# Kernel tuning notes

Measured on AMD Instinct MI355X. Metric: run time of the kernel, lower is better.

The kernel has to match this reference:

```python
import jax, jax.numpy as jnp
import numpy as np

B, S, DIM, HID = 2, 256, 128, 128
EPS = 1e-5

def _ln(t, w, b):
    mu = jnp.mean(t, axis=-1, keepdims=True)
    var = jnp.mean(jnp.square(t - mu), axis=-1, keepdims=True)
    return (t - mu) * jax.lax.rsqrt(var + EPS) * w + b

def setup_inputs() -> dict:
    key = jax.random.key(0)
    ks = jax.random.split(key, 8)
    sc = 1.0 / np.sqrt(DIM)
    return {
        "x": jax.random.normal(ks[0], (B, S, S, DIM), dtype=jnp.float32),
        "mask": jax.random.uniform(ks[1], (B, S, S), dtype=jnp.float32),
        "norm_w": jnp.ones((DIM,), jnp.float32),
        "norm_b": jnp.zeros((DIM,), jnp.float32),
        "w_left": jax.random.uniform(ks[2], (HID, DIM), jnp.float32, -sc, sc),
        "w_right": jax.random.uniform(ks[3], (HID, DIM), jnp.float32, -sc, sc),
        "w_lg": jax.random.uniform(ks[4], (HID, DIM), jnp.float32, -sc, sc),
        "w_rg": jax.random.uniform(ks[5], (HID, DIM), jnp.float32, -sc, sc),
        "w_og": jax.random.uniform(ks[6], (HID, DIM), jnp.float32, -sc, sc),
        "out_norm_w": jnp.ones((HID,), jnp.float32),
        "out_norm_b": jnp.zeros((HID,), jnp.float32),
        "w_out": jax.random.uniform(ks[7], (DIM, HID), jnp.float32, -1.0 / np.sqrt(HID), 1.0 / np.sqrt(HID)),
    }

def reference(x, mask, norm_w, norm_b, w_left, w_right, w_lg, w_rg, w_og,
              out_norm_w, out_norm_b, w_out):
    xn = _ln(x, norm_w, norm_b)                      # [B,S,S,D]
    m = mask[..., None]                              # [B,S,S,1]
    left = (xn @ w_left.T) * m * jax.nn.sigmoid(xn @ w_lg.T)    # [B,S,S,H]
    right = (xn @ w_right.T) * m * jax.nn.sigmoid(xn @ w_rg.T)  # [B,S,S,H]
    out_gate = jax.nn.sigmoid(xn @ w_og.T)
    # torch: permute to [B,H,S,S], bf16 bmm, permute back -> out[b,i,j,h] = sum_k L[b,i,k,h]*R[b,j,k,h]
    out = jnp.einsum("bikh,bjkh->bijh",
                     left.astype(jnp.bfloat16), right.astype(jnp.bfloat16),
                     preferred_element_type=jnp.float32)
    out = out.astype(jnp.bfloat16).astype(jnp.float32)
    out = _ln(out, out_norm_w, out_norm_b) * out_gate
    return out @ w_out.T                             # [B,S,S,D]
```

## Files before the change

kernel.cpp:

```cpp
#include <hip/hip_runtime.h>


#define SS 256
#define DD 128
#define HH 128

typedef __attribute__((ext_vector_type(8))) short bf16x8;
typedef __attribute__((ext_vector_type(4))) float f32x4;

__device__ __forceinline__ unsigned short f2b(float f) {
  unsigned u = __builtin_bit_cast(unsigned, f);
  u = (u + 0x7FFFu + ((u >> 16) & 1u)) >> 16;
  return (unsigned short)u;
}
__device__ __forceinline__ float b2f(unsigned short h) {
  return __builtin_bit_cast(float, ((unsigned)h) << 16);
}
__device__ __forceinline__ float sigmoidf_(float x) {
  return 1.0f / (1.0f + expf(-x));
}

__global__ __launch_bounds__(1024) void k_cvt(
    const float* __restrict__ s0, const float* __restrict__ s1,
    const float* __restrict__ s2, const float* __restrict__ s3,
    const float* __restrict__ s4, const float* __restrict__ s5,
    unsigned short* __restrict__ dst)
{
  int m = blockIdx.x >> 4;
  int e = ((blockIdx.x & 15) << 10) | threadIdx.x;
  const float* s = (m == 0) ? s0 : (m == 1) ? s1 : (m == 2) ? s2
                 : (m == 3) ? s3 : (m == 4) ? s4 : s5;
  dst[m * 16384 + e] = f2b(s[e]);
}

__global__ __launch_bounds__(256, 4) void k_stage1(
    const float* __restrict__ x, const float* __restrict__ mask,
    const float* __restrict__ nw, const float* __restrict__ nb,
    const unsigned short* __restrict__ wb,
    unsigned short* __restrict__ Lt, unsigned short* __restrict__ Rt,
    unsigned short* __restrict__ og)
{
  __shared__ unsigned short xnS[64][136];
  __shared__ unsigned short oS[128][72];
  __shared__ float maskS[64];

  const int tid  = threadIdx.x;
  const int wave = tid >> 6, lane = tid & 63;
  const int quad = lane >> 4, l16 = lane & 15;
  const int r0 = blockIdx.x * 64;
  const int bq = r0 >> 16, iq = (r0 >> 8) & 255, j0 = r0 & 255;

  if (tid < 64) maskS[tid] = mask[r0 + tid];

  const float w0 = nw[lane], w1 = nw[lane + 64];
  const float b0 = nb[lane], b1 = nb[lane + 64];
  float v0a[16], v1a[16];
  #pragma unroll
  for (int rr = 0; rr < 16; ++rr) {
    const float* xr = x + (size_t)(r0 + wave * 16 + rr) * DD;
    v0a[rr] = xr[lane];
    v1a[rr] = xr[lane + 64];
  }
  #pragma unroll
  for (int rr = 0; rr < 16; ++rr) {
    int r = wave * 16 + rr;
    float v0 = v0a[rr], v1 = v1a[rr];
    float s = v0 + v1;
    #pragma unroll
    for (int o = 32; o; o >>= 1) s += __shfl_xor(s, o);
    float mu = s * (1.0f / 128.0f);
    float d0 = v0 - mu, d1 = v1 - mu;
    float q = d0 * d0 + d1 * d1;
    #pragma unroll
    for (int o = 32; o; o >>= 1) q += __shfl_xor(q, o);
    float rs = rsqrtf(q * (1.0f / 128.0f) + 1e-5f);
    xnS[r][lane]      = f2b(d0 * rs * w0 + b0);
    xnS[r][lane + 64] = f2b(d1 * rs * w1 + b1);
  }
  __syncthreads();

  const int h0 = wave * 32;
  const int jl = quad * 4;

  auto coopStore = [&](unsigned short* dstBase) {
    int h = tid >> 1, half = tid & 1;
    const bf16x8* s = (const bf16x8*)&oS[h][half * 32];
    bf16x8* d = (bf16x8*)(dstBase +
        ((((size_t)bq * 128 + h) * 256 + iq) * 256 + j0 + half * 32));
    d[0] = s[0]; d[1] = s[1]; d[2] = s[2]; d[3] = s[3];
  };

  auto gatedSection = [&](const unsigned short* __restrict__ Wv,
                          const unsigned short* __restrict__ Wg) {
    const unsigned short* pv = Wv + (h0 + l16) * 128 + quad * 8;
    const unsigned short* pg = Wg + (h0 + l16) * 128 + quad * 8;
    f32x4 aV[4][2], aG[4][2];
    #pragma unroll
    for (int rt = 0; rt < 4; ++rt)
      #pragma unroll
      for (int n = 0; n < 2; ++n) {
        aV[rt][n] = f32x4{0.f, 0.f, 0.f, 0.f};
        aG[rt][n] = f32x4{0.f, 0.f, 0.f, 0.f};
      }
    bf16x8 bv[2], bg[2], bvn[2], bgn[2];
    #pragma unroll
    for (int n = 0; n < 2; ++n) {
      bv[n] = *(const bf16x8*)(pv + n * 2048);
      bg[n] = *(const bf16x8*)(pg + n * 2048);
    }
    #pragma unroll
    for (int kk = 0; kk < 4; ++kk) {
      if (kk < 3) {
        #pragma unroll
        for (int n = 0; n < 2; ++n) {
          bvn[n] = *(const bf16x8*)(pv + n * 2048 + (kk + 1) * 32);
          bgn[n] = *(const bf16x8*)(pg + n * 2048 + (kk + 1) * 32);
        }
      }
      #pragma unroll
      for (int rt = 0; rt < 4; ++rt) {
        bf16x8 a = *(const bf16x8*)&xnS[rt * 16 + l16][kk * 32 + quad * 8];
        #pragma unroll
        for (int n = 0; n < 2; ++n) {
          aG[rt][n] = __builtin_amdgcn_mfma_f32_16x16x32_bf16(a, bg[n], aG[rt][n], 0, 0, 0);
          aV[rt][n] = __builtin_amdgcn_mfma_f32_16x16x32_bf16(a, bv[n], aV[rt][n], 0, 0, 0);
        }
      }
      #pragma unroll
      for (int n = 0; n < 2; ++n) { bv[n] = bvn[n]; bg[n] = bgn[n]; }
    }
    #pragma unroll
    for (int rt = 0; rt < 4; ++rt)
      #pragma unroll
      for (int n = 0; n < 2; ++n)
        #pragma unroll
        for (int rg = 0; rg < 4; ++rg) {
          float g = sigmoidf_(aG[rt][n][rg]);
          oS[h0 + n * 16 + l16][rt * 16 + jl + rg] =
              f2b(aV[rt][n][rg] * maskS[rt * 16 + jl + rg] * g);
        }
  };

  gatedSection(wb + 0 * 16384, wb + 2 * 16384);
  __syncthreads();
  coopStore(Lt);
  __syncthreads();

  gatedSection(wb + 1 * 16384, wb + 3 * 16384);
  __syncthreads();
  coopStore(Rt);
  __syncthreads();

  {
    const unsigned short* po = wb + 4 * 16384 + (h0 + l16) * 128 + quad * 8;
    f32x4 aO[4][2];
    #pragma unroll
    for (int rt = 0; rt < 4; ++rt)
      #pragma unroll
      for (int n = 0; n < 2; ++n) aO[rt][n] = f32x4{0.f, 0.f, 0.f, 0.f};
    bf16x8 bo[2], bon[2];
    #pragma unroll
    for (int n = 0; n < 2; ++n) bo[n] = *(const bf16x8*)(po + n * 2048);
    #pragma unroll
    for (int kk = 0; kk < 4; ++kk) {
      if (kk < 3) {
        #pragma unroll
        for (int n = 0; n < 2; ++n)
          bon[n] = *(const bf16x8*)(po + n * 2048 + (kk + 1) * 32);
      }
      #pragma unroll
      for (int rt = 0; rt < 4; ++rt) {
        bf16x8 a = *(const bf16x8*)&xnS[rt * 16 + l16][kk * 32 + quad * 8];
        #pragma unroll
        for (int n = 0; n < 2; ++n)
          aO[rt][n] = __builtin_amdgcn_mfma_f32_16x16x32_bf16(a, bo[n], aO[rt][n], 0, 0, 0);
      }
      #pragma unroll
      for (int n = 0; n < 2; ++n) bo[n] = bon[n];
    }
    unsigned short* ogS = &oS[0][0];
    #pragma unroll
    for (int rt = 0; rt < 4; ++rt)
      #pragma unroll
      for (int n = 0; n < 2; ++n)
        #pragma unroll
        for (int rg = 0; rg < 4; ++rg)
          ogS[(rt * 16 + jl + rg) * 136 + h0 + n * 16 + l16] =
              f2b(sigmoidf_(aO[rt][n][rg]));
  }
  __syncthreads();
  {
    int j = tid >> 2, qq = tid & 3;
    const unsigned short* ogS = &oS[0][0];
    const bf16x8* sp = (const bf16x8*)&ogS[j * 136 + qq * 32];
    bf16x8* d = (bf16x8*)(og + (size_t)(r0 + j) * HH + qq * 32);
    d[0] = sp[0]; d[1] = sp[1]; d[2] = sp[2]; d[3] = sp[3];
  }
}

__global__ __launch_bounds__(256, 4) void k_stage2(
    const unsigned short* __restrict__ Lt, const unsigned short* __restrict__ Rt,
    unsigned short* __restrict__ Tt)
{
  __shared__ unsigned short As[128][72];
  __shared__ unsigned short Bs[128][72];

  const int tid  = threadIdx.x;
  const int wave = tid >> 6, lane = tid & 63;
  const int quad = lane >> 4, l16 = lane & 15;

  const int w   = blockIdx.y * 4 + blockIdx.x;
  const int grp = w >> 4;
  const int xcd = w & 7;
  const int jt  = (w >> 3) & 1;
  const int pid = grp * 8 + xcd;
  const int bh  = pid >> 1;
  const int it  = pid & 1;

  const unsigned short* A  = Lt + (size_t)bh * 65536 + it * 128 * 256;
  const unsigned short* Bp = Rt + (size_t)bh * 65536 + jt * 128 * 256;

  f32x4 acc[2][8];
  #pragma unroll
  for (int mt = 0; mt < 2; ++mt)
    #pragma unroll
    for (int nt = 0; nt < 8; ++nt) acc[mt][nt] = f32x4{0.f, 0.f, 0.f, 0.f};

  const int srow = tid >> 3, sc8 = tid & 7;

  bf16x8 ra[4], rb[4];
  #pragma unroll
  for (int i = 0; i < 4; ++i) {
    ra[i] = *(const bf16x8*)(A  + (i * 32 + srow) * 256 + sc8 * 8);
    rb[i] = *(const bf16x8*)(Bp + (i * 32 + srow) * 256 + sc8 * 8);
  }

  #pragma unroll
  for (int ks = 0; ks < 4; ++ks) {
    #pragma unroll
    for (int i = 0; i < 4; ++i) {
      *(bf16x8*)&As[i * 32 + srow][sc8 * 8] = ra[i];
      *(bf16x8*)&Bs[i * 32 + srow][sc8 * 8] = rb[i];
    }
    __syncthreads();
    if (ks < 3) {
      #pragma unroll
      for (int i = 0; i < 4; ++i) {
        ra[i] = *(const bf16x8*)(A  + (i * 32 + srow) * 256 + (ks + 1) * 64 + sc8 * 8);
        rb[i] = *(const bf16x8*)(Bp + (i * 32 + srow) * 256 + (ks + 1) * 64 + sc8 * 8);
      }
    }
    #pragma unroll
    for (int k2 = 0; k2 < 2; ++k2) {
      int ko = k2 * 32 + quad * 8;
      bf16x8 a0 = *(const bf16x8*)&As[wave * 32 + l16][ko];
      bf16x8 a1 = *(const bf16x8*)&As[wave * 32 + 16 + l16][ko];
      #pragma unroll
      for (int nt = 0; nt < 8; ++nt) {
        bf16x8 b = *(const bf16x8*)&Bs[nt * 16 + l16][ko];
        acc[0][nt] = __builtin_amdgcn_mfma_f32_16x16x32_bf16(a0, b, acc[0][nt], 0, 0, 0);
        acc[1][nt] = __builtin_amdgcn_mfma_f32_16x16x32_bf16(a1, b, acc[1][nt], 0, 0, 0);
      }
    }
    __syncthreads();
  }

  unsigned short* C = Tt + (size_t)bh * 65536 + it * 128 * 256 + jt * 128;
  #pragma unroll
  for (int mt = 0; mt < 2; ++mt)
    #pragma unroll
    for (int nt = 0; nt < 8; ++nt)
      #pragma unroll
      for (int rg = 0; rg < 4; ++rg)
        C[(wave * 32 + mt * 16 + quad * 4 + rg) * 256 + nt * 16 + l16] = f2b(acc[mt][nt][rg]);
}

__global__ __launch_bounds__(256, 4) void k_stage3(
    const unsigned short* __restrict__ Tt, const unsigned short* __restrict__ og,
    const float* __restrict__ onw, const float* __restrict__ onb,
    const unsigned short* __restrict__ wbO, float* __restrict__ out)
{
  __shared__ unsigned short tS[128][72];
  __shared__ unsigned short vS[64][136];
  __shared__ float onwS[128], onbS[128];

  const int tid  = threadIdx.x;
  const int wave = tid >> 6, lane = tid & 63;
  const int quad = lane >> 4, l16 = lane & 15;
  const int r0 = blockIdx.x * 64;
  const int bq = r0 >> 16, iq = (r0 >> 8) & 255, j0 = r0 & 255;
  const int jw = wave * 16;

  const int jE = jw + (lane >> 2), hq = lane & 3;
  bf16x8 gpre[4];
  {
    const unsigned short* ogp = og + (size_t)(r0 + jE) * HH + hq * 32;
    #pragma unroll
    for (int c = 0; c < 4; ++c) gpre[c] = *(const bf16x8*)(ogp + c * 8);
  }

  if (tid < 128) { onwS[tid] = onw[tid]; onbS[tid] = onb[tid]; }

  {
    int h = tid >> 1, half = tid & 1;
    const bf16x8* s = (const bf16x8*)(Tt +
        ((((size_t)bq * 128 + h) * 256 + iq) * 256 + j0 + half * 32));
    bf16x8* d = (bf16x8*)&tS[h][half * 32];
    d[0] = s[0]; d[1] = s[1]; d[2] = s[2]; d[3] = s[3];
  }
  __syncthreads();

  {
    int j = jw + (lane & 15);
    int hb = (lane >> 4) * 32;
    #pragma unroll
    for (int c = 0; c < 4; ++c) {
      bf16x8 t;
      #pragma unroll
      for (int e = 0; e < 8; ++e) t[e] = (short)tS[hb + c * 8 + e][j];
      *(bf16x8*)&vS[j][hb + c * 8] = t;
    }
  }
  asm volatile("s_waitcnt lgkmcnt(0)" ::: "memory");

  float mu, rs;
  {
    int j = jw + ((lane & 31) >> 1), h0 = (lane & 1) * 64;
    float s = 0.f, q = 0.f;
    #pragma unroll
    for (int c = 0; c < 8; ++c) {
      bf16x8 v8 = *(const bf16x8*)&vS[j][h0 + c * 8];
      #pragma unroll
      for (int e = 0; e < 8; ++e) {
        float v = b2f((unsigned short)v8[e]);
        s += v; q += v * v;
      }
    }
    s += __shfl_xor(s, 1);
    q += __shfl_xor(q, 1);
    mu = s * (1.0f / 128.0f);
    float var = q * (1.0f / 128.0f) - mu * mu;
    rs = rsqrtf(var + 1e-5f);
  }
  mu = __shfl(mu, (jE - jw) << 1);
  rs = __shfl(rs, (jE - jw) << 1);

  {
    unsigned short* vp = &vS[jE][hq * 32];
    #pragma unroll
    for (int c = 0; c < 4; ++c) {
      bf16x8 tv = *(bf16x8*)&vp[c * 8];
      bf16x8 gv = gpre[c];
      bf16x8 r;
      #pragma unroll
      for (int e = 0; e < 8; ++e) {
        int hh = hq * 32 + c * 8 + e;
        float v = (b2f((unsigned short)tv[e]) - mu) * rs * onwS[hh] + onbS[hh];
        r[e] = (short)f2b(v * b2f((unsigned short)gv[e]));
      }
      *(bf16x8*)&vp[c * 8] = r;
    }
  }
  asm volatile("s_waitcnt lgkmcnt(0)" ::: "memory");

  f32x4 acc[8];
  #pragma unroll
  for (int nt = 0; nt < 8; ++nt) acc[nt] = f32x4{0.f, 0.f, 0.f, 0.f};
  #pragma unroll
  for (int kk = 0; kk < 4; ++kk) {
    bf16x8 a = *(const bf16x8*)&vS[jw + l16][kk * 32 + quad * 8];
    #pragma unroll
    for (int nt = 0; nt < 8; ++nt) {
      bf16x8 b = *(const bf16x8*)(wbO + (nt * 16 + l16) * 128 + kk * 32 + quad * 8);
      acc[nt] = __builtin_amdgcn_mfma_f32_16x16x32_bf16(a, b, acc[nt], 0, 0, 0);
    }
  }
  #pragma unroll
  for (int nt = 0; nt < 8; ++nt)
    #pragma unroll
    for (int rg = 0; rg < 4; ++rg)
      out[(size_t)(r0 + jw + quad * 4 + rg) * DD + nt * 16 + l16] = acc[nt][rg];
}

extern "C" void kernel_launch(void* const* d_in, const int* in_sizes, int n_in,
                              void* d_out, int out_size, void* d_ws, size_t ws_size,
                              hipStream_t stream)
{
  const float* x    = (const float*)d_in[0];
  const float* mask = (const float*)d_in[1];
  const float* nw   = (const float*)d_in[2];
  const float* nb   = (const float*)d_in[3];
  const float* wL   = (const float*)d_in[4];
  const float* wR   = (const float*)d_in[5];
  const float* wLG  = (const float*)d_in[6];
  const float* wRG  = (const float*)d_in[7];
  const float* wOG  = (const float*)d_in[8];
  const float* onw  = (const float*)d_in[9];
  const float* onb  = (const float*)d_in[10];
  const float* wO   = (const float*)d_in[11];

  char* ws = (char*)d_ws;
  unsigned short* wb = (unsigned short*)ws;
  unsigned short* og = (unsigned short*)(ws + (1 << 18));
  unsigned short* Lt = (unsigned short*)(ws + (1 << 18) + 1 * (size_t)(1 << 25));
  unsigned short* Rt = (unsigned short*)(ws + (1 << 18) + 2 * (size_t)(1 << 25));
  unsigned short* Tt = (unsigned short*)(ws + (1 << 18) + 3 * (size_t)(1 << 25));

  k_cvt<<<96, 1024, 0, stream>>>(wL, wR, wLG, wRG, wOG, wO, wb);
  k_stage1<<<2048, 256, 0, stream>>>(x, mask, nw, nb, wb, Lt, Rt, og);
  k_stage2<<<dim3(4, 256), 256, 0, stream>>>(Lt, Rt, Tt);
  k_stage3<<<2048, 256, 0, stream>>>(Tt, og, onw, onb, wb + 5 * 16384, (float*)d_out);
}
```

Baseline: 276.1 us.

## Vectorize stores via swapped MFMA operands, swizzle transpose LDS, overlap stage1 sections

Several MFMA calls swap their A and B operands so each lane's accumulator holds contiguous output elements. That lets the epilogues write packed bf16x4 or f32x4 vectors instead of scattered scalar stores, in stage1's og path, stage2's C store and stage3's output. Stage3's transpose buffer gets an XOR swizzle to cut LDS bank conflicts. Stage1 now runs the second gated GEMM before the barrier that protects the shared output buffer, which removes one barrier and overlaps compute with the previous store. The weight conversion kernel is vectorized to four elements per thread. The cost is more complex index math and a higher risk of layout mistakes.

```diff
diff --git a/kernel.cpp b/kernel.cpp
--- a/kernel.cpp
+++ b/kernel.cpp
@@ -6,6 +6,7 @@
 #define HH 128
 
 typedef __attribute__((ext_vector_type(8))) short bf16x8;
+typedef __attribute__((ext_vector_type(4))) short bf16x4;
 typedef __attribute__((ext_vector_type(4))) float f32x4;
 
 __device__ __forceinline__ unsigned short f2b(float f) {
@@ -26,11 +27,15 @@
     const float* __restrict__ s4, const float* __restrict__ s5,
     unsigned short* __restrict__ dst)
 {
-  int m = blockIdx.x >> 4;
-  int e = ((blockIdx.x & 15) << 10) | threadIdx.x;
+  int m = blockIdx.x >> 2;
+  int e4 = (((blockIdx.x & 3) << 10) | threadIdx.x) << 2;
   const float* s = (m == 0) ? s0 : (m == 1) ? s1 : (m == 2) ? s2
                  : (m == 3) ? s3 : (m == 4) ? s4 : s5;
-  dst[m * 16384 + e] = f2b(s[e]);
+  f32x4 v = *(const f32x4*)(s + e4);
+  bf16x4 r;
+  #pragma unroll
+  for (int i = 0; i < 4; ++i) r[i] = (short)f2b(v[i]);
+  *(bf16x4*)(dst + m * 16384 + e4) = r;
 }
 
 __global__ __launch_bounds__(256, 4) void k_stage1(
@@ -90,11 +95,11 @@
     d[0] = s[0]; d[1] = s[1]; d[2] = s[2]; d[3] = s[3];
   };
 
-  auto gatedSection = [&](const unsigned short* __restrict__ Wv,
-                          const unsigned short* __restrict__ Wg) {
+  auto gatedCompute = [&](const unsigned short* __restrict__ Wv,
+                          const unsigned short* __restrict__ Wg,
+                          f32x4 (&aV)[4][2], f32x4 (&aG)[4][2]) {
     const unsigned short* pv = Wv + (h0 + l16) * 128 + quad * 8;
     const unsigned short* pg = Wg + (h0 + l16) * 128 + quad * 8;
-    f32x4 aV[4][2], aG[4][2];
     #pragma unroll
     for (int rt = 0; rt < 4; ++rt)
       #pragma unroll
@@ -129,27 +134,34 @@
       #pragma unroll
       for (int n = 0; n < 2; ++n) { bv[n] = bvn[n]; bg[n] = bgn[n]; }
     }
+  };
+
+  auto gatedEpilogue = [&](f32x4 (&aV)[4][2], f32x4 (&aG)[4][2]) {
     #pragma unroll
     for (int rt = 0; rt < 4; ++rt)
       #pragma unroll
-      for (int n = 0; n < 2; ++n)
+      for (int n = 0; n < 2; ++n) {
+        bf16x4 p;
         #pragma unroll
         for (int rg = 0; rg < 4; ++rg) {
           float g = sigmoidf_(aG[rt][n][rg]);
-          oS[h0 + n * 16 + l16][rt * 16 + jl + rg] =
-              f2b(aV[rt][n][rg] * maskS[rt * 16 + jl + rg] * g);
+          p[rg] = (short)f2b(aV[rt][n][rg] * maskS[rt * 16 + jl + rg] * g);
         }
+        *(bf16x4*)&oS[h0 + n * 16 + l16][rt * 16 + jl] = p;
+      }
   };
 
-  gatedSection(wb + 0 * 16384, wb + 2 * 16384);
+  f32x4 aV[4][2], aG[4][2];
+
+  gatedCompute(wb + 0 * 16384, wb + 2 * 16384, aV, aG);
+  gatedEpilogue(aV, aG);
   __syncthreads();
   coopStore(Lt);
-  __syncthreads();
-
-  gatedSection(wb + 1 * 16384, wb + 3 * 16384);
+  gatedCompute(wb + 1 * 16384, wb + 3 * 16384, aV, aG);
+  __syncthreads();
+  gatedEpilogue(aV, aG);
   __syncthreads();
   coopStore(Rt);
-  __syncthreads();
 
   {
     const unsigned short* po = wb + 4 * 16384 + (h0 + l16) * 128 + quad * 8;
@@ -173,20 +185,23 @@
         bf16x8 a = *(const bf16x8*)&xnS[rt * 16 + l16][kk * 32 + quad * 8];
         #pragma unroll
         for (int n = 0; n < 2; ++n)
-          aO[rt][n] = __builtin_amdgcn_mfma_f32_16x16x32_bf16(a, bo[n], aO[rt][n], 0, 0, 0);
+          aO[rt][n] = __builtin_amdgcn_mfma_f32_16x16x32_bf16(bo[n], a, aO[rt][n], 0, 0, 0);
       }
       #pragma unroll
       for (int n = 0; n < 2; ++n) bo[n] = bon[n];
     }
+    __syncthreads();
     unsigned short* ogS = &oS[0][0];
     #pragma unroll
     for (int rt = 0; rt < 4; ++rt)
       #pragma unroll
-      for (int n = 0; n < 2; ++n)
+      for (int n = 0; n < 2; ++n) {
+        bf16x4 p;
         #pragma unroll
         for (int rg = 0; rg < 4; ++rg)
-          ogS[(rt * 16 + jl + rg) * 136 + h0 + n * 16 + l16] =
-              f2b(sigmoidf_(aO[rt][n][rg]));
+          p[rg] = (short)f2b(sigmoidf_(aO[rt][n][rg]));
+        *(bf16x4*)&ogS[(rt * 16 + l16) * 136 + h0 + n * 16 + quad * 4] = p;
+      }
   }
   __syncthreads();
   {
@@ -253,13 +268,13 @@
     #pragma unroll
     for (int k2 = 0; k2 < 2; ++k2) {
       int ko = k2 * 32 + quad * 8;
-      bf16x8 a0 = *(const bf16x8*)&As[wave * 32 + l16][ko];
-      bf16x8 a1 = *(const bf16x8*)&As[wave * 32 + 16 + l16][ko];
+      bf16x8 r0f = *(const bf16x8*)&Bs[wave * 32 + l16][ko];
+      bf16x8 r1f = *(const bf16x8*)&Bs[wave * 32 + 16 + l16][ko];
       #pragma unroll
       for (int nt = 0; nt < 8; ++nt) {
-        bf16x8 b = *(const bf16x8*)&Bs[nt * 16 + l16][ko];
-        acc[0][nt] = __builtin_amdgcn_mfma_f32_16x16x32_bf16(a0, b, acc[0][nt], 0, 0, 0);
-        acc[1][nt] = __builtin_amdgcn_mfma_f32_16x16x32_bf16(a1, b, acc[1][nt], 0, 0, 0);
+        bf16x8 lf = *(const bf16x8*)&As[nt * 16 + l16][ko];
+        acc[0][nt] = __builtin_amdgcn_mfma_f32_16x16x32_bf16(r0f, lf, acc[0][nt], 0, 0, 0);
+        acc[1][nt] = __builtin_amdgcn_mfma_f32_16x16x32_bf16(r1f, lf, acc[1][nt], 0, 0, 0);
       }
     }
     __syncthreads();
@@ -269,10 +284,12 @@
   #pragma unroll
   for (int mt = 0; mt < 2; ++mt)
     #pragma unroll
-    for (int nt = 0; nt < 8; ++nt)
-      #pragma unroll
-      for (int rg = 0; rg < 4; ++rg)
-        C[(wave * 32 + mt * 16 + quad * 4 + rg) * 256 + nt * 16 + l16] = f2b(acc[mt][nt][rg]);
+    for (int nt = 0; nt < 8; ++nt) {
+      bf16x4 p;
+      #pragma unroll
+      for (int rg = 0; rg < 4; ++rg) p[rg] = (short)f2b(acc[mt][nt][rg]);
+      *(bf16x4*)&C[(nt * 16 + l16) * 256 + wave * 32 + mt * 16 + quad * 4] = p;
+    }
 }
 
 __global__ __launch_bounds__(256, 4) void k_stage3(
@@ -303,21 +320,25 @@
 
   {
     int h = tid >> 1, half = tid & 1;
+    int g = (h >> 5) & 3;
     const bf16x8* s = (const bf16x8*)(Tt +
         ((((size_t)bq * 128 + h) * 256 + iq) * 256 + j0 + half * 32));
-    bf16x8* d = (bf16x8*)&tS[h][half * 32];
-    d[0] = s[0]; d[1] = s[1]; d[2] = s[2]; d[3] = s[3];
-  }
-  __syncthreads();
-
-  {
-    int j = jw + (lane & 15);
+    #pragma unroll
+    for (int c = 0; c < 4; ++c)
+      *(bf16x8*)&tS[h][((half * 4 + c) ^ g) << 3] = s[c];
+  }
+  __syncthreads();
+
+  {
+    int j  = jw + (lane & 15);
+    int g2 = (lane >> 4) & 3;
     int hb = (lane >> 4) * 32;
+    int jc = (((j >> 3) ^ g2) << 3) | (j & 7);
     #pragma unroll
     for (int c = 0; c < 4; ++c) {
       bf16x8 t;
       #pragma unroll
-      for (int e = 0; e < 8; ++e) t[e] = (short)tS[hb + c * 8 + e][j];
+      for (int e = 0; e < 8; ++e) t[e] = (short)tS[hb + c * 8 + e][jc];
       *(bf16x8*)&vS[j][hb + c * 8] = t;
     }
   }
@@ -368,18 +389,16 @@
   for (int nt = 0; nt < 8; ++nt) acc[nt] = f32x4{0.f, 0.f, 0.f, 0.f};
   #pragma unroll
   for (int kk = 0; kk < 4; ++kk) {
-    bf16x8 a = *(const bf16x8*)&vS[jw + l16][kk * 32 + quad * 8];
+    bf16x8 xv = *(const bf16x8*)&vS[jw + l16][kk * 32 + quad * 8];
     #pragma unroll
     for (int nt = 0; nt < 8; ++nt) {
-      bf16x8 b = *(const bf16x8*)(wbO + (nt * 16 + l16) * 128 + kk * 32 + quad * 8);
-      acc[nt] = __builtin_amdgcn_mfma_f32_16x16x32_bf16(a, b, acc[nt], 0, 0, 0);
+      bf16x8 wv = *(const bf16x8*)(wbO + (nt * 16 + l16) * 128 + kk * 32 + quad * 8);
+      acc[nt] = __builtin_amdgcn_mfma_f32_16x16x32_bf16(wv, xv, acc[nt], 0, 0, 0);
     }
   }
   #pragma unroll
   for (int nt = 0; nt < 8; ++nt)
-    #pragma unroll
-    for (int rg = 0; rg < 4; ++rg)
-      out[(size_t)(r0 + jw + quad * 4 + rg) * DD + nt * 16 + l16] = acc[nt][rg];
+    *(f32x4*)&out[(size_t)(r0 + jw + l16) * DD + nt * 16 + quad * 4] = acc[nt];
 }
 
 extern "C" void kernel_launch(void* const* d_in, const int* in_sizes, int n_in,
@@ -406,7 +425,7 @@
   unsigned short* Rt = (unsigned short*)(ws + (1 << 18) + 2 * (size_t)(1 << 25));
   unsigned short* Tt = (unsigned short*)(ws + (1 << 18) + 3 * (size_t)(1 << 25));
 
-  k_cvt<<<96, 1024, 0, stream>>>(wL, wR, wLG, wRG, wOG, wO, wb);
+  k_cvt<<<24, 1024, 0, stream>>>(wL, wR, wLG, wRG, wOG, wO, wb);
   k_stage1<<<2048, 256, 0, stream>>>(x, mask, nw, nb, wb, Lt, Rt, og);
   k_stage2<<<dim3(4, 256), 256, 0, stream>>>(Lt, Rt, Tt);
   k_stage3<<<2048, 256, 0, stream>>>(Tt, og, onw, onb, wb + 5 * 16384, (float*)d_out);
```

Result: faster. 267.8 us (median of 2 runs) (-3.0%).
